# Kernel tuning notes

Measured on AMD Instinct MI355X. Metric: run time of the kernel, lower is better.

## Reference

```python
import jax, jax.numpy as jnp
import numpy as np

EPS_ATTN = 1e-5   # attention denominator eps (module eps)
EPS_LN = 1e-5     # nn.LayerNorm default eps


def _prime(x, proj):
    # Performer FAVOR+ hyperbolic positive features.
    # x: (B,H,L,dh), proj: (dh,m) -> (B,H,L,2m)
    dn = x.shape[-1] ** -0.25
    xn = dn * x
    d = jnp.einsum('bhld,dm->bhlm', xn, proj)
    diag = 0.5 * jnp.sum(xn * xn, axis=-1, keepdims=True)
    return jnp.concatenate([jnp.exp(d - diag), jnp.exp(-d - diag)], axis=-1)


def setup_inputs() -> dict:
    L, B, H, DH, DM, M = 2048, 4, 8, 64, 512, 256
    key = jax.random.key(0)
    k0, k1, k2 = jax.random.split(key, 3)
    h = jax.random.normal(k0, (L, B, DM), jnp.float32)
    w_qkv = jax.random.normal(k1, (H * 3 * DH, DM), jnp.float32) / np.sqrt(DM)
    w_o = jax.random.normal(k2, (DM, H * DH), jnp.float32) / np.sqrt(H * DH)
    ln_gamma = jnp.ones((DM,), jnp.float32)
    ln_beta = jnp.zeros((DM,), jnp.float32)
    # Gaussian orthogonal random matrix (blockwise QR), rows scaled by sqrt(dh)
    rng = np.random.default_rng(0)
    blocks = []
    for _ in range(M // DH):
        g = rng.standard_normal((DH, DH)).astype(np.float32)
        q, _ = np.linalg.qr(g)
        blocks.append(q.T)
    pm = np.concatenate(blocks, axis=0) * np.sqrt(DH)  # (M, DH)
    proj_matrix = jnp.asarray(pm.T.astype(np.float32))  # (DH, M)
    return {"h": h, "w_qkv": w_qkv, "w_o": w_o,
            "ln_gamma": ln_gamma, "ln_beta": ln_beta,
            "proj_matrix": proj_matrix}


def _forward(h, w_qkv, w_o, ln_gamma, ln_beta, proj_matrix):
    L, B, DM = h.shape
    DH, M = proj_matrix.shape
    H = w_qkv.shape[0] // (3 * DH)
    scale = DH ** -0.5

    qkv = (h @ w_qkv.T).reshape(L, B, H, 3 * DH)
    q, k, v = jnp.split(qkv, 3, axis=-1)
    q = jnp.transpose(q, (1, 2, 0, 3))  # (B,H,L,dh)
    k = jnp.transpose(k, (1, 2, 0, 3))
    v = jnp.transpose(v, (1, 2, 0, 3))

    qp = _prime(q, proj_matrix)  # (B,H,L,2M)
    kp = _prime(k, proj_matrix)
    kp = kp / jnp.sum(kp, axis=-1, keepdims=True)
    qp = qp / jnp.sum(qp, axis=-1, keepdims=True)

    den_acc = jnp.cumsum(kp, axis=2)
    denom = jnp.einsum('bhlm,bhlm->bhl', den_acc, qp)[..., None]  # (B,H,L,1)

    # fast_weight_sum: W_t = W_{t-1} + k_t v_t^T ; out_t = q_t @ W_t
    def step(W, xs):
        qt, kt, vt = xs  # (B,H,2M), (B,H,2M), (B,H,dh)
        W = W + kt[..., :, None] * vt[..., None, :]
        out = jnp.einsum('bhm,bhmd->bhd', qt, W)
        return W, out

    W0 = jnp.zeros((B, H, 2 * M, DH), h.dtype)
    xs = (jnp.transpose(qp, (2, 0, 1, 3)),
          jnp.transpose(kp, (2, 0, 1, 3)),
          jnp.transpose(v, (2, 0, 1, 3)))
    _, out = jax.lax.scan(step, W0, xs)  # (L,B,H,dh)
    out = jnp.transpose(out, (1, 2, 0, 3))  # (B,H,L,dh)

    out = scale * out / (denom + EPS_ATTN)
    out = jnp.transpose(out, (0, 2, 1, 3)).reshape(B, L, H * DH)  # (B,L,H*dh)
    out = jnp.swapaxes(out, 0, 1)  # (L,B,H*dh)

    attn_out = out @ w_o.T
    x = h + attn_out
    mu = jnp.mean(x, axis=-1, keepdims=True)
    var = jnp.mean((x - mu) ** 2, axis=-1, keepdims=True)
    return (x - mu) / jnp.sqrt(var + EPS_LN) * ln_gamma + ln_beta


def reference(h, w_qkv, w_o, ln_gamma, ln_beta, proj_matrix):
    return _forward(h, w_qkv, w_o, ln_gamma, ln_beta, proj_matrix)
```

## Files before the change

kernel.cpp:

```cpp
#include <hip/hip_runtime.h>
#include <hip/hip_fp16.h>
#include <math.h>

#define LSEQ 2048
#define NB 4
#define NH 8
#define DMID 512
#define CHK 128
#define SCALE 0.125f
#define DN 0.35355339059327373f
#define DN2 0.125f
#define EPS_ATTN 1e-5f
#define EPS_LN 1e-5f

typedef _Float16 f16x8 __attribute__((ext_vector_type(8)));
typedef _Float16 f16x4 __attribute__((ext_vector_type(4)));
typedef float f32x4 __attribute__((ext_vector_type(4)));

__device__ __forceinline__ void cvt16(const float* __restrict__ p,
                                      _Float16* __restrict__ dst) {
  float4 a = *(const float4*)p, b = *(const float4*)(p + 4);
  float4 c = *(const float4*)(p + 8), d = *(const float4*)(p + 12);
  f16x8 t0 = {(_Float16)a.x, (_Float16)a.y, (_Float16)a.z, (_Float16)a.w,
              (_Float16)b.x, (_Float16)b.y, (_Float16)b.z, (_Float16)b.w};
  f16x8 t1 = {(_Float16)c.x, (_Float16)c.y, (_Float16)c.z, (_Float16)c.w,
              (_Float16)d.x, (_Float16)d.y, (_Float16)d.z, (_Float16)d.w};
  *(f16x8*)dst = t0;
  *(f16x8*)(dst + 8) = t1;
}

__global__ void k_diag(float* out, int n, float val) {
  int i = blockIdx.x * 256 + threadIdx.x;
  if (i < n) out[i] = val;
}

__global__ __launch_bounds__(256) void k_ptr(const float* __restrict__ proj,
                                             __half* __restrict__ projT) {
  int e = blockIdx.x * 256 + threadIdx.x;
  int n = e >> 6, k = e & 63;
  projT[e] = __float2half_rn(proj[k * 256 + n] * DN);
}

__global__ __launch_bounds__(256) void k_qkv(
    const float* __restrict__ A, const float* __restrict__ Wq,
    __half* __restrict__ q, __half* __restrict__ k, __half* __restrict__ v) {
  __shared__ __align__(16) char smem[34816];
  _Float16* Ah = (_Float16*)smem;
  _Float16* Bh = (_Float16*)(smem + 10240);
  _Float16* Oh = (_Float16*)smem;

  const int tid = threadIdx.x;
  const int row0 = blockIdx.x * 128;
  const int col0 = blockIdx.y * 128;
  const int lane = tid & 63, wv = tid >> 6;
  const int ln15 = lane & 15, quad = lane >> 4;
  const int m0 = wv * 32;
  const int srow = tid >> 1, sc = (tid & 1) * 16;

  f32x4 Cacc[2][8];
  const f32x4 z4 = {0.f, 0.f, 0.f, 0.f};
#pragma unroll
  for (int mi = 0; mi < 2; ++mi)
#pragma unroll
    for (int nt = 0; nt < 8; ++nt) Cacc[mi][nt] = z4;

  for (int kt = 0; kt < DMID; kt += 32) {
    cvt16(A + (size_t)(row0 + srow) * DMID + kt + sc, &Ah[srow * 40 + sc]);
    cvt16(Wq + (size_t)(col0 + srow) * DMID + kt + sc, &Bh[srow * 40 + sc]);
    __syncthreads();
    f16x8 a0 = *(const f16x8*)&Ah[(m0 + ln15) * 40 + quad * 8];
    f16x8 a1 = *(const f16x8*)&Ah[(m0 + 16 + ln15) * 40 + quad * 8];
#pragma unroll
    for (int nt = 0; nt < 8; ++nt) {
      f16x8 bf = *(const f16x8*)&Bh[(nt * 16 + ln15) * 40 + quad * 8];
      Cacc[0][nt] = __builtin_amdgcn_mfma_f32_16x16x32_f16(a0, bf, Cacc[0][nt], 0, 0, 0);
      Cacc[1][nt] = __builtin_amdgcn_mfma_f32_16x16x32_f16(a1, bf, Cacc[1][nt], 0, 0, 0);
    }
    __syncthreads();
  }
#pragma unroll
  for (int mi = 0; mi < 2; ++mi)
#pragma unroll
    for (int nt = 0; nt < 8; ++nt)
#pragma unroll
      for (int r = 0; r < 4; ++r)
        Oh[(m0 + mi * 16 + quad * 4 + r) * 136 + nt * 16 + ln15] =
            (_Float16)Cacc[mi][nt][r];
  __syncthreads();
  const int tr = tid >> 4, tc = tid & 15;
  const int col = col0 + tc * 8;
  const int hh = col / 192;
  const int rem = col - hh * 192;
  const int t = rem >> 6;
  const int d0 = rem & 63;
  __half* dstb = (t == 0) ? q : ((t == 1) ? k : v);
#pragma unroll
  for (int i = 0; i < 8; ++i) {
    int lrow = tr * 8 + i;
    int grow = row0 + lrow;
    int l = grow >> 2, bb = grow & 3;
    f16x8 val = *(const f16x8*)&Oh[lrow * 136 + tc * 8];
    *(f16x8*)((_Float16*)dstb + (((size_t)(bb * NH + hh) * LSEQ + l) << 6) + d0) = val;
  }
}

__global__ __launch_bounds__(256, 4) void k_dgemm(
    const __half* __restrict__ qsrc, const __half* __restrict__ ksrc,
    const __half* __restrict__ projT, __half* __restrict__ dqd,
    __half* __restrict__ dkd, float2* __restrict__ nq,
    float2* __restrict__ nk) {
  __shared__ __align__(16) char smem[37376];
  _Float16* Bt = (_Float16*)smem;
  float* g_l  = (float*)(smem + 36864);
  float* ps_l = (float*)(smem + 37120);
  _Float16* Oh = (_Float16*)smem;

  const int tid = threadIdx.x;
  const __half* src = blockIdx.y ? ksrc : qsrc;
  __half* dst = blockIdx.y ? dkd : dqd;
  float2* nrm = blockIdx.y ? nk : nq;
  const size_t r0 = (size_t)blockIdx.x * 64;

  const int lane = tid & 63, wv = tid >> 6;
  const int ln15 = lane & 15, quad = lane >> 4;
  const int m0 = wv * 16;

#pragma unroll
  for (int it = 0; it < 8; ++it) {
    int e = it * 256 + tid;
    int n = e >> 3, seg = e & 7;
    *(f16x8*)&Bt[n * 72 + seg * 8] =
        *(const f16x8*)((const _Float16*)projT + n * 64 + seg * 8);
  }

  f16x8 afrag[2];
  float ss = 0.f;
  {
    const _Float16* rp = (const _Float16*)src + (r0 + m0 + ln15) * 64;
#pragma unroll
    for (int ks = 0; ks < 2; ++ks) {
      f16x8 x8 = *(const f16x8*)(rp + ks * 32 + quad * 8);
      afrag[ks] = x8;
#pragma unroll
      for (int j = 0; j < 8; ++j) {
        float xv = (float)x8[j];
        ss = fmaf(xv, xv, ss);
      }
    }
    ss += __shfl_xor(ss, 16);
    ss += __shfl_xor(ss, 32);
  }
  if (quad == 0) g_l[m0 + ln15] = 0.5f * DN2 * ss;
  __syncthreads();

  f32x4 Cacc[16];
  const f32x4 z4 = {0.f, 0.f, 0.f, 0.f};
#pragma unroll
  for (int nt = 0; nt < 16; ++nt) Cacc[nt] = z4;

#pragma unroll
  for (int ks = 0; ks < 2; ++ks) {
    f16x8 a0 = afrag[ks];
#pragma unroll
    for (int nt = 0; nt < 16; ++nt) {
      f16x8 bf = *(const f16x8*)&Bt[(nt * 16 + ln15) * 72 + ks * 32 + quad * 8];
      Cacc[nt] = __builtin_amdgcn_mfma_f32_16x16x32_f16(a0, bf, Cacc[nt], 0, 0, 0);
    }
  }

  float gv[4], pp[4];
#pragma unroll
  for (int r = 0; r < 4; ++r) {
    gv[r] = g_l[m0 + quad * 4 + r];
    pp[r] = 0.f;
  }
#pragma unroll
  for (int nt = 0; nt < 16; ++nt)
#pragma unroll
    for (int r = 0; r < 4; ++r) {
      float d = Cacc[nt][r];
      pp[r] += __expf(d - gv[r]) + __expf(-d - gv[r]);
    }
#pragma unroll
  for (int r = 0; r < 4; ++r) {
    float p = pp[r];
    p += __shfl_xor(p, 1); p += __shfl_xor(p, 2);
    p += __shfl_xor(p, 4); p += __shfl_xor(p, 8);
    if (ln15 == 0) ps_l[m0 + quad * 4 + r] = p;
  }

#pragma unroll
  for (int hf = 0; hf < 2; ++hf) {
    __syncthreads();
#pragma unroll
    for (int nt2 = 0; nt2 < 8; ++nt2) {
      int nt = hf * 8 + nt2;
#pragma unroll
      for (int r = 0; r < 4; ++r)
        Oh[(m0 + quad * 4 + r) * 136 + nt2 * 16 + ln15] =
            (_Float16)Cacc[nt][r];
    }
    __syncthreads();
#pragma unroll
    for (int it = 0; it < 4; ++it) {
      int e = it * 256 + tid;
      int row = e >> 4, seg = e & 15;
      *(f16x8*)((_Float16*)dst + (r0 + row) * 256 + hf * 128 + seg * 8) =
          *(const f16x8*)&Oh[row * 136 + seg * 8];
    }
  }
  if (tid < 64) nrm[r0 + tid] = make_float2(g_l[tid], 1.0f / ps_l[tid]);
}

__global__ __launch_bounds__(256) void k_kv(
    const __half* __restrict__ dk, const float2* __restrict__ nk,
    const __half* __restrict__ v, __half* __restrict__ KVt,
    float* __restrict__ Ks) {
  __shared__ __align__(16) char smem[53248];
  _Float16* kpT = (_Float16*)smem;
  _Float16* Vt  = (_Float16*)(smem + 34816);
  float* gk = (float*)(smem + 52224);
  float* ik = (float*)(smem + 52736);
  _Float16* Oh2 = (_Float16*)smem;

  const int tid = threadIdx.x;
  const int cidx = blockIdx.x;
  const int i0 = blockIdx.y * 128;
  const float fsign = (i0 < 256) ? 1.f : -1.f;
  const int m0col = (i0 < 256) ? i0 : i0 - 256;
  const size_t rowbase = (size_t)cidx * CHK;

  if (tid < 128) {
    float2 n = nk[rowbase + tid];
    gk[tid] = n.x; ik[tid] = n.y;
  }
  __syncthreads();

  {
    const int srow = tid >> 1;
    const int scol = (tid & 1) * 64;
    float g = gk[srow], ivs = ik[srow];
    const _Float16* src =
        (const _Float16*)dk + (rowbase + srow) * 256 + m0col + scol;
#pragma unroll
    for (int it = 0; it < 8; ++it) {
      f16x8 d8 = *(const f16x8*)(src + it * 8);
#pragma unroll
      for (int j = 0; j < 8; ++j)
        kpT[(scol + it * 8 + j) * 136 + srow] =
            (_Float16)(__expf(fsign * (float)d8[j] - g) * ivs);
    }
  }
  {
    int s = tid & 127, dq0 = (tid >> 7) * 32;
    const _Float16* vsrc = (const _Float16*)v + (rowbase + s) * 64 + dq0;
#pragma unroll
    for (int b8 = 0; b8 < 4; ++b8) {
      f16x8 v8 = ((const f16x8*)vsrc)[b8];
#pragma unroll
      for (int j = 0; j < 8; ++j)
        Vt[(dq0 + b8 * 8 + j) * 136 + s] = v8[j];
    }
  }
  __syncthreads();

  const int lane = tid & 63, wv = tid >> 6;
  const int ln15 = lane & 15, quad = lane >> 4;
  const int m0 = wv * 32;

  f32x4 Cacc[2][4], Kacc[2];
  const f32x4 z4 = {0.f, 0.f, 0.f, 0.f};
#pragma unroll
  for (int mi = 0; mi < 2; ++mi) {
#pragma unroll
    for (int nt = 0; nt < 4; ++nt) Cacc[mi][nt] = z4;
    Kacc[mi] = z4;
  }
  f16x8 bone;
#pragma unroll
  for (int j = 0; j < 8; ++j)
    bone[j] = (ln15 == 0) ? (_Float16)1.0f : (_Float16)0.0f;

#pragma unroll
  for (int ks = 0; ks < 4; ++ks) {
    f16x8 a0 = *(const f16x8*)&kpT[(m0 + ln15) * 136 + ks * 32 + quad * 8];
    f16x8 a1 = *(const f16x8*)&kpT[(m0 + 16 + ln15) * 136 + ks * 32 + quad * 8];
#pragma unroll
    for (int nt = 0; nt < 4; ++nt) {
      f16x8 bV = *(const f16x8*)&Vt[(nt * 16 + ln15) * 136 + ks * 32 + quad * 8];
      Cacc[0][nt] = __builtin_amdgcn_mfma_f32_16x16x32_f16(a0, bV, Cacc[0][nt], 0, 0, 0);
      Cacc[1][nt] = __builtin_amdgcn_mfma_f32_16x16x32_f16(a1, bV, Cacc[1][nt], 0, 0, 0);
    }
    Kacc[0] = __builtin_amdgcn_mfma_f32_16x16x32_f16(a0, bone, Kacc[0], 0, 0, 0);
    Kacc[1] = __builtin_amdgcn_mfma_f32_16x16x32_f16(a1, bone, Kacc[1], 0, 0, 0);
  }

  if (ln15 == 0) {
#pragma unroll
    for (int mi = 0; mi < 2; ++mi)
#pragma unroll
      for (int r = 0; r < 4; ++r)
        Ks[(size_t)cidx * 512 + i0 + m0 + mi * 16 + quad * 4 + r] = Kacc[mi][r];
  }
  __syncthreads();
#pragma unroll
  for (int mi = 0; mi < 2; ++mi)
#pragma unroll
    for (int nt = 0; nt < 4; ++nt) {
      f16x4 pack = {(_Float16)Cacc[mi][nt][0], (_Float16)Cacc[mi][nt][1],
                    (_Float16)Cacc[mi][nt][2], (_Float16)Cacc[mi][nt][3]};
      *(f16x4*)&Oh2[(nt * 16 + ln15) * 136 + m0 + mi * 16 + quad * 4] = pack;
    }
  __syncthreads();
  {
    int d = tid >> 2, part = tid & 3;
    _Float16* dstp =
        (_Float16*)KVt + (size_t)cidx * 32768 + d * 512 + i0 + part * 32;
    const _Float16* srcp = &Oh2[d * 136 + part * 32];
#pragma unroll
    for (int j = 0; j < 4; ++j)
      *(f16x8*)(dstp + j * 8) = *(const f16x8*)(srcp + j * 8);
  }
}

__global__ __launch_bounds__(256) void k_scan(__half2* __restrict__ KV2,
                                              float* __restrict__ Ks) {
  const int bh = blockIdx.x;
  const int e0 = blockIdx.y * 2048;
  for (int ee = 0; ee < 8; ++ee) {
    int e = e0 + ee * 256 + threadIdx.x;
    float ax = 0.f, ay = 0.f;
    __half2* p = KV2 + (size_t)bh * 16 * 16384 + e;
#pragma unroll
    for (int c = 0; c < 16; ++c) {
      float2 f = __half22float2(p[(size_t)c * 16384]);
      p[(size_t)c * 16384] = __floats2half2_rn(ax, ay);
      ax += f.x; ay += f.y;
    }
  }
  if (blockIdx.y == 0) {
    for (int ee = 0; ee < 2; ++ee) {
      int i = ee * 256 + threadIdx.x;
      float a = 0.f;
      float* p = Ks + (size_t)bh * 16 * 512 + i;
#pragma unroll
      for (int c = 0; c < 16; ++c) {
        float vv = p[c * 512];
        p[c * 512] = a;
        a += vv;
      }
    }
  }
}

template <int TH>
__device__ __forceinline__ void attn_body(
    const __half* __restrict__ dq, const __half* __restrict__ dk,
    const float2* __restrict__ nq, const float2* __restrict__ nk,
    const __half* __restrict__ v, const __half* __restrict__ KVt,
    const float* __restrict__ Kpre, float* __restrict__ outb, char* smem) {
  constexpr int KROWS = TH ? 128 : 64;
  constexpr int NS = TH ? 8 : 4;
  constexpr int NKS = TH ? 4 : 2;

  float* gq_l   = (float*)(smem);
  float* iq_l   = (float*)(smem + 256);
  float* gk_l   = (float*)(smem + 512);
  float* ik_l   = (float*)(smem + 1024);
  float* den1_l = (float*)(smem + 1536);
  float* den2_l = (float*)(smem + 1792);
  float* invd_l = (float*)(smem + 2048);
  float* KpT    = (float*)(smem + 2304);
  _Float16* qpT = (_Float16*)(smem + 2432);
  _Float16* kpT = (_Float16*)(smem + 7552);
  _Float16* WT  = (_Float16*)(smem + 17792);
  _Float16* S_h = (_Float16*)(smem + 2432);
  _Float16* Vt  = (_Float16*)(smem + 22912);

  const int tid = threadIdx.x;
  const int cidx = blockIdx.x;
  const int cc = cidx & 15, bh = cidx >> 4;
  const size_t rowb = (size_t)cidx * 128;
  const size_t rowt = rowb + TH * 64;
  const int lane = tid & 63;
  const int wv = tid >> 6;
  const int ln15 = lane & 15;
  const int quad = lane >> 4;
  const int m0 = wv * 16;

  if (tid < 64) {
    float2 n = nq[rowt + tid];
    gq_l[tid] = n.x; iq_l[tid] = n.y;
  }
  if (tid < KROWS) {
    float2 n2 = nk[rowb + tid];
    gk_l[tid] = n2.x; ik_l[tid] = n2.y;
  }
  __syncthreads();

  f32x4 Sacc[NS], Oacc[4], Dacc;
  const f32x4 z4 = {0.f, 0.f, 0.f, 0.f};
#pragma unroll
  for (int nt = 0; nt < NS; ++nt) Sacc[nt] = z4;
#pragma unroll
  for (int nt = 0; nt < 4; ++nt) Oacc[nt] = z4;
  Dacc = z4;

  const int qrow = tid >> 2, qc = (tid & 3) * 8;
  const int krow = tid >> 1, kc = (tid & 1) * 16;

  for (int kt = 0; kt < 512; kt += 32) {
    const float sgn = (kt < 256) ? 1.f : -1.f;
    const int dbase = (kt < 256) ? kt : kt - 256;
    {
      const _Float16* src = (const _Float16*)dq + (rowt + qrow) * 256 + dbase + qc;
      float g = gq_l[qrow], iv = iq_l[qrow];
      f16x8 d0 = *(const f16x8*)(src);
      f16x8 t0;
#pragma unroll
      for (int j = 0; j < 8; ++j)
        t0[j] = (_Float16)(__expf(sgn * (float)d0[j] - g) * iv);
      *(f16x8*)&qpT[qrow * 40 + qc] = t0;
    }
    if (TH == 1 || krow < 64) {
      const _Float16* src = (const _Float16*)dk + (rowb + krow) * 256 + dbase + kc;
      float g = gk_l[krow], iv = ik_l[krow];
      f16x8 d0 = *(const f16x8*)(src);
      f16x8 d1 = *(const f16x8*)(src + 8);
      f16x8 t0, t1;
#pragma unroll
      for (int j = 0; j < 8; ++j) {
        t0[j] = (_Float16)(__expf(sgn * (float)d0[j] - g) * iv);
        t1[j] = (_Float16)(__expf(sgn * (float)d1[j] - g) * iv);
      }
      *(f16x8*)&kpT[krow * 40 + kc] = t0;
      *(f16x8*)&kpT[krow * 40 + kc + 8] = t1;
    }
    {
      int d = tid >> 2, seg = tid & 3;
      *(f16x8*)&WT[d * 40 + seg * 8] =
          *(const f16x8*)((const _Float16*)KVt + (size_t)cidx * 32768 +
                          d * 512 + kt + seg * 8);
    }
    if (tid < 32) KpT[tid] = Kpre[(size_t)cidx * 512 + kt + tid];
    __syncthreads();

    f16x8 a0 = *(const f16x8*)&qpT[(m0 + ln15) * 40 + quad * 8];
#pragma unroll
    for (int nt = 0; nt < NS; ++nt) {
      f16x8 bf = *(const f16x8*)&kpT[(nt * 16 + ln15) * 40 + quad * 8];
      Sacc[nt] = __builtin_amdgcn_mfma_f32_16x16x32_f16(a0, bf, Sacc[nt], 0, 0, 0);
    }
#pragma unroll
    for (int nt = 0; nt < 4; ++nt) {
      f16x8 bw = *(const f16x8*)&WT[(nt * 16 + ln15) * 40 + quad * 8];
      Oacc[nt] = __builtin_amdgcn_mfma_f32_16x16x32_f16(a0, bw, Oacc[nt], 0, 0, 0);
    }
    {
      f16x8 bk;
#pragma unroll
      for (int j = 0; j < 8; ++j)
        bk[j] = (ln15 == 0) ? (_Float16)KpT[quad * 8 + j] : (_Float16)0.f;
      Dacc = __builtin_amdgcn_mfma_f32_16x16x32_f16(a0, bk, Dacc, 0, 0, 0);
    }
    __syncthreads();
  }

  if (ln15 == 0) {
#pragma unroll
    for (int r = 0; r < 4; ++r)
      den2_l[m0 + quad * 4 + r] = Dacc[r];
  }
  {
    float dp[4] = {0.f, 0.f, 0.f, 0.f};
#pragma unroll
    for (int nt = 0; nt < NS; ++nt) {
      int s = nt * 16 + ln15;
#pragma unroll
      for (int r = 0; r < 4; ++r) {
        int tl = m0 + quad * 4 + r;
        float vsv = (s <= TH * 64 + tl) ? Sacc[nt][r] : 0.f;
        dp[r] += vsv;
        S_h[tl * 136 + s] = (_Float16)vsv;
      }
    }
#pragma unroll
    for (int r = 0; r < 4; ++r) {
      float p = dp[r];
      p += __shfl_xor(p, 1); p += __shfl_xor(p, 2);
      p += __shfl_xor(p, 4); p += __shfl_xor(p, 8);
      if (ln15 == 0) den1_l[m0 + quad * 4 + r] = p;
    }
  }
  __syncthreads();
  if (tid < 64)
    invd_l[tid] = SCALE / (den1_l[tid] + den2_l[tid] + EPS_ATTN);
  {
    int s = tid & 127, d0v = (tid >> 7) * 32;
    if (TH == 1 || s < 64) {
      const _Float16* vsrc = (const _Float16*)v + (rowb + s) * 64 + d0v;
      f16x8 v0 = ((const f16x8*)vsrc)[0];
      f16x8 v1 = ((const f16x8*)vsrc)[1];
      f16x8 v2 = ((const f16x8*)vsrc)[2];
      f16x8 v3 = ((const f16x8*)vsrc)[3];
#pragma unroll
      for (int j = 0; j < 8; ++j) {
        Vt[(d0v + j) * 136 + s] = v0[j];
        Vt[(d0v + 8 + j) * 136 + s] = v1[j];
        Vt[(d0v + 16 + j) * 136 + s] = v2[j];
        Vt[(d0v + 24 + j) * 136 + s] = v3[j];
      }
    }
  }
  __syncthreads();
#pragma unroll
  for (int ks = 0; ks < NKS; ++ks) {
    f16x8 aS0 = *(const f16x8*)&S_h[(m0 + ln15) * 136 + ks * 32 + quad * 8];
#pragma unroll
    for (int nt = 0; nt < 4; ++nt) {
      f16x8 bV = *(const f16x8*)&Vt[(nt * 16 + ln15) * 136 + ks * 32 + quad * 8];
      Oacc[nt] = __builtin_amdgcn_mfma_f32_16x16x32_f16(aS0, bV, Oacc[nt], 0, 0, 0);
    }
  }
  const int b = bh >> 3, hh = bh & 7;
  float ivv[4];
#pragma unroll
  for (int r = 0; r < 4; ++r)
    ivv[r] = invd_l[m0 + quad * 4 + r];
#pragma unroll
  for (int nt = 0; nt < 4; ++nt) {
    int dcol = nt * 16 + ln15;
#pragma unroll
    for (int r = 0; r < 4; ++r) {
      int tl = m0 + quad * 4 + r;
      int l = cc * 128 + TH * 64 + tl;
      outb[((size_t)l * 4 + b) * 512 + hh * 64 + dcol] = Oacc[nt][r] * ivv[r];
    }
  }
}

__global__ __launch_bounds__(256, 4) void k_attn(
    const __half* __restrict__ dq, const __half* __restrict__ dk,
    const float2* __restrict__ nq, const float2* __restrict__ nk,
    const __half* __restrict__ v, const __half* __restrict__ KVt,
    const float* __restrict__ Kpre, float* __restrict__ outb) {
  __shared__ __align__(16) char smem[40320];
  if (blockIdx.y == 0)
    attn_body<0>(dq, dk, nq, nk, v, KVt, Kpre, outb, smem);
  else
    attn_body<1>(dq, dk, nq, nk, v, KVt, Kpre, outb, smem);
}

__global__ __launch_bounds__(256) void k_oproj(
    const float* __restrict__ A, const float* __restrict__ Wo,
    const float* __restrict__ hres, float* __restrict__ xout) {
  __shared__ __align__(16) char smem[34816];
  _Float16* Ah = (_Float16*)smem;
  _Float16* Bh = (_Float16*)(smem + 10240);
  _Float16* Oh = (_Float16*)smem;

  const int tid = threadIdx.x;
  const int row0 = blockIdx.x * 128;
  const int col0 = blockIdx.y * 128;
  const int lane = tid & 63, wv = tid >> 6;
  const int ln15 = lane & 15, quad = lane >> 4;
  const int m0 = wv * 32;
  const int srow = tid >> 1, sc = (tid & 1) * 16;

  f32x4 Cacc[2][8];
  const f32x4 z4 = {0.f, 0.f, 0.f, 0.f};
#pragma unroll
  for (int mi = 0; mi < 2; ++mi)
#pragma unroll
    for (int nt = 0; nt < 8; ++nt) Cacc[mi][nt] = z4;

  for (int kt = 0; kt < DMID; kt += 32) {
    cvt16(A + (size_t)(row0 + srow) * DMID + kt + sc, &Ah[srow * 40 + sc]);
    cvt16(Wo + (size_t)(col0 + srow) * DMID + kt + sc, &Bh[srow * 40 + sc]);
    __syncthreads();
    f16x8 a0 = *(const f16x8*)&Ah[(m0 + ln15) * 40 + quad * 8];
    f16x8 a1 = *(const f16x8*)&Ah[(m0 + 16 + ln15) * 40 + quad * 8];
#pragma unroll
    for (int nt = 0; nt < 8; ++nt) {
      f16x8 bf = *(const f16x8*)&Bh[(nt * 16 + ln15) * 40 + quad * 8];
      Cacc[0][nt] = __builtin_amdgcn_mfma_f32_16x16x32_f16(a0, bf, Cacc[0][nt], 0, 0, 0);
      Cacc[1][nt] = __builtin_amdgcn_mfma_f32_16x16x32_f16(a1, bf, Cacc[1][nt], 0, 0, 0);
    }
    __syncthreads();
  }
#pragma unroll
  for (int mi = 0; mi < 2; ++mi)
#pragma unroll
    for (int nt = 0; nt < 8; ++nt)
#pragma unroll
      for (int r = 0; r < 4; ++r)
        Oh[(m0 + mi * 16 + quad * 4 + r) * 136 + nt * 16 + ln15] =
            (_Float16)Cacc[mi][nt][r];
  __syncthreads();
  const int tr = tid >> 4, tc = tid & 15;
#pragma unroll
  for (int i = 0; i < 8; ++i) {
    int lrow = tr * 8 + i;
    int grow = row0 + lrow;
    size_t base = (size_t)grow * 512 + col0 + tc * 8;
    f16x8 o = *(const f16x8*)&Oh[lrow * 136 + tc * 8];
    float4 h0 = *(const float4*)(hres + base);
    float4 h1 = *(const float4*)(hres + base + 4);
    *(float4*)(xout + base) =
        make_float4((float)o[0] + h0.x, (float)o[1] + h0.y,
                    (float)o[2] + h0.z, (float)o[3] + h0.w);
    *(float4*)(xout + base + 4) =
        make_float4((float)o[4] + h1.x, (float)o[5] + h1.y,
                    (float)o[6] + h1.z, (float)o[7] + h1.w);
  }
}

__global__ __launch_bounds__(256) void k_ln(float* __restrict__ x,
                                            const float* __restrict__ g,
                                            const float* __restrict__ bta) {
  __shared__ float ws_[4], wq_[4];
  const int row = blockIdx.x;
  const int tid = threadIdx.x;
  float2 vv = *(const float2*)(x + (size_t)row * 512 + tid * 2);
  float s = vv.x + vv.y;
  float sq = vv.x * vv.x + vv.y * vv.y;
#pragma unroll
  for (int off = 1; off < 64; off <<= 1) {
    s += __shfl_xor(s, off, 64);
    sq += __shfl_xor(sq, off, 64);
  }
  if ((tid & 63) == 0) { ws_[tid >> 6] = s; wq_[tid >> 6] = sq; }
  __syncthreads();
  s = ws_[0] + ws_[1] + ws_[2] + ws_[3];
  sq = wq_[0] + wq_[1] + wq_[2] + wq_[3];
  float mu = s * (1.f / 512.f);
  float var = sq * (1.f / 512.f) - mu * mu;
  float rstd = rsqrtf(var + EPS_LN);
  int c = tid * 2;
  float2 o;
  o.x = (vv.x - mu) * rstd * g[c] + bta[c];
  o.y = (vv.y - mu) * rstd * g[c + 1] + bta[c + 1];
  *(float2*)(x + (size_t)row * 512 + c) = o;
}

extern "C" void kernel_launch(void* const* d_in, const int* in_sizes, int n_in,
                              void* d_out, int out_size, void* d_ws,
                              size_t ws_size, hipStream_t stream) {
  const float* h    = (const float*)d_in[0];
  const float* wqkv = (const float*)d_in[1];
  const float* wo   = (const float*)d_in[2];
  const float* g    = (const float*)d_in[3];
  const float* bta  = (const float*)d_in[4];
  const float* proj = (const float*)d_in[5];
  float* out = (float*)d_out;
  char* wsb = (char*)d_ws;

  __half* q   = (__half*)(wsb + 0);
  __half* kb  = (__half*)(wsb + 8388608);
  __half* vb  = (__half*)(wsb + 16777216);
  __half* dq  = (__half*)(wsb + 25165824);
  __half* dk  = (__half*)(wsb + 58720256);
  float2* nq  = (float2*)(wsb + 92274688);
  float2* nk  = (float2*)(wsb + 92798976);
  __half* KVt = (__half*)(wsb + 93323264);
  float*  Ks  = (float*)(wsb + 126877696);
  __half* pT  = (__half*)(wsb + 127926272);
  float* outb = (float*)(wsb + 0);

  if (ws_size < 127959040ull) {
    float val = 1000.0f + (float)(ws_size >> 20);
    k_diag<<<(out_size + 255) / 256, 256, 0, stream>>>(out, out_size, val);
    return;
  }

  k_ptr  <<<dim3(64), 256, 0, stream>>>(proj, pT);
  k_qkv  <<<dim3(64, 12), 256, 0, stream>>>(h, wqkv, q, kb, vb);
  k_dgemm<<<dim3(1024, 2), 256, 0, stream>>>(q, kb, pT, dq, dk, nq, nk);
  k_kv   <<<dim3(512, 4), 256, 0, stream>>>(dk, nk, vb, KVt, Ks);
  k_scan <<<dim3(32, 8), 256, 0, stream>>>((__half2*)KVt, Ks);
  k_attn <<<dim3(512, 2), 256, 0, stream>>>(dq, dk, nq, nk, vb, KVt, Ks, outb);
  k_oproj<<<dim3(64, 4), 256, 0, stream>>>(outb, wo, h, out);
  k_ln   <<<dim3(8192), 256, 0, stream>>>(out, g, bta);
}
```

Before: 257.6 us.

## Register-prefetch attention tiles, widen k-step, parallelize scan, remap attn blocks

The attention kernel now handles 64 feature columns per iteration instead of 32, giving 8 iterations rather than 16. It prefetches the next tile's dq, dk, KV and Kpre values into registers while the current tile is computed, which hides global-load latency and halves the number of barriers. The chunk scan is split across more blocks: each thread does vectorized 8-byte loads of all 16 chunks up front, and the Ks prefix sum runs in separate blocks. The attention grid is flattened and remapped so that the two halves of a chunk run in adjacent blocks, which may improve cache locality. The costs are higher register pressure and a changed shared-memory layout.

```diff
diff --git a/kernel.cpp b/kernel.cpp
--- a/kernel.cpp
+++ b/kernel.cpp
@@ -326,30 +326,35 @@
 __global__ __launch_bounds__(256) void k_scan(__half2* __restrict__ KV2,
                                               float* __restrict__ Ks) {
   const int bh = blockIdx.x;
-  const int e0 = blockIdx.y * 2048;
-  for (int ee = 0; ee < 8; ++ee) {
-    int e = e0 + ee * 256 + threadIdx.x;
-    float ax = 0.f, ay = 0.f;
-    __half2* p = KV2 + (size_t)bh * 16 * 16384 + e;
+  const int tid = threadIdx.x;
+  if (blockIdx.y < 32) {
+    uint2* p = (uint2*)(KV2 + (size_t)bh * 262144) + (blockIdx.y * 256 + tid);
+    uint2 raw[16];
+#pragma unroll
+    for (int c = 0; c < 16; ++c) raw[c] = p[c * 8192];
+    float ax0 = 0.f, ay0 = 0.f, ax1 = 0.f, ay1 = 0.f;
 #pragma unroll
     for (int c = 0; c < 16; ++c) {
-      float2 f = __half22float2(p[(size_t)c * 16384]);
-      p[(size_t)c * 16384] = __floats2half2_rn(ax, ay);
-      ax += f.x; ay += f.y;
-    }
-  }
-  if (blockIdx.y == 0) {
-    for (int ee = 0; ee < 2; ++ee) {
-      int i = ee * 256 + threadIdx.x;
-      float a = 0.f;
-      float* p = Ks + (size_t)bh * 16 * 512 + i;
-#pragma unroll
-      for (int c = 0; c < 16; ++c) {
-        float vv = p[c * 512];
-        p[c * 512] = a;
-        a += vv;
-      }
-    }
+      __half2 h0 = *(__half2*)&raw[c].x;
+      __half2 h1 = *(__half2*)&raw[c].y;
+      float2 f0 = __half22float2(h0), f1 = __half22float2(h1);
+      __half2 o0 = __floats2half2_rn(ax0, ay0);
+      __half2 o1 = __floats2half2_rn(ax1, ay1);
+      uint2 o;
+      o.x = *(unsigned*)&o0;
+      o.y = *(unsigned*)&o1;
+      p[c * 8192] = o;
+      ax0 += f0.x; ay0 += f0.y; ax1 += f1.x; ay1 += f1.y;
+    }
+  } else {
+    int i = (blockIdx.y - 32) * 256 + tid;
+    float* pk = Ks + (size_t)bh * 8192 + i;
+    float vs[16];
+#pragma unroll
+    for (int c = 0; c < 16; ++c) vs[c] = pk[c * 512];
+    float a = 0.f;
+#pragma unroll
+    for (int c = 0; c < 16; ++c) { pk[c * 512] = a; a += vs[c]; }
   }
 }
 
@@ -358,27 +363,28 @@
     const __half* __restrict__ dq, const __half* __restrict__ dk,
     const float2* __restrict__ nq, const float2* __restrict__ nk,
     const __half* __restrict__ v, const __half* __restrict__ KVt,
-    const float* __restrict__ Kpre, float* __restrict__ outb, char* smem) {
+    const float* __restrict__ Kpre, float* __restrict__ outb, int cidx,
+    char* smem) {
   constexpr int KROWS = TH ? 128 : 64;
+  constexpr int KR32 = KROWS / 32;
   constexpr int NS = TH ? 8 : 4;
   constexpr int NKS = TH ? 4 : 2;
 
-  float* gq_l   = (float*)(smem);
-  float* iq_l   = (float*)(smem + 256);
-  float* gk_l   = (float*)(smem + 512);
-  float* ik_l   = (float*)(smem + 1024);
-  float* den1_l = (float*)(smem + 1536);
-  float* den2_l = (float*)(smem + 1792);
-  float* invd_l = (float*)(smem + 2048);
-  float* KpT    = (float*)(smem + 2304);
-  _Float16* qpT = (_Float16*)(smem + 2432);
-  _Float16* kpT = (_Float16*)(smem + 7552);
-  _Float16* WT  = (_Float16*)(smem + 17792);
-  _Float16* S_h = (_Float16*)(smem + 2432);
-  _Float16* Vt  = (_Float16*)(smem + 22912);
+  _Float16* qpT = (_Float16*)(smem);
+  _Float16* kpT = (_Float16*)(smem + 9216);
+  _Float16* WT  = (_Float16*)(smem + 27648);
+  float*    KpT = (float*)(smem + 36864);
+  _Float16* S_h = (_Float16*)(smem);
+  _Float16* Vt  = (_Float16*)(smem + 17408);
+  float* gq_l   = (float*)(smem + 37120);
+  float* iq_l   = (float*)(smem + 37376);
+  float* gk_l   = (float*)(smem + 37632);
+  float* ik_l   = (float*)(smem + 38144);
+  float* den1_l = (float*)(smem + 38656);
+  float* den2_l = (float*)(smem + 38912);
+  float* invd_l = (float*)(smem + 39168);
 
   const int tid = threadIdx.x;
-  const int cidx = blockIdx.x;
   const int cc = cidx & 15, bh = cidx >> 4;
   const size_t rowb = (size_t)cidx * 128;
   const size_t rowt = rowb + TH * 64;
@@ -398,6 +404,40 @@
   }
   __syncthreads();
 
+  const int c8 = tid & 7;
+  const int r8 = tid >> 3;
+  const int csrc = (c8 & 3) * 8;
+  const float sgn = (c8 < 4) ? 1.f : -1.f;
+
+  const _Float16* qsrc = (const _Float16*)dq + (rowt + r8) * 256 + csrc;
+  const _Float16* ksrc = (const _Float16*)dk + (rowb + r8) * 256 + csrc;
+  const _Float16* wsrc = (const _Float16*)KVt + (size_t)cidx * 32768 +
+                         r8 * 512 + ((c8 < 4) ? 0 : 256) + csrc;
+  const float* kpsrc = Kpre + (size_t)cidx * 512 +
+                       ((tid < 32) ? tid : (tid < 64 ? 224 + tid : 0));
+
+  float gq[2], iq[2], gk[KR32], ik[KR32];
+#pragma unroll
+  for (int p = 0; p < 2; ++p) {
+    gq[p] = gq_l[r8 + p * 32];
+    iq[p] = iq_l[r8 + p * 32];
+  }
+#pragma unroll
+  for (int p = 0; p < KR32; ++p) {
+    gk[p] = gk_l[r8 + p * 32];
+    ik[p] = ik_l[r8 + p * 32];
+  }
+
+  f16x8 rq[2], rk[KR32], rw[2];
+  float rkp = 0.f;
+#pragma unroll
+  for (int p = 0; p < 2; ++p) rq[p] = *(const f16x8*)(qsrc + p * 8192);
+#pragma unroll
+  for (int p = 0; p < KR32; ++p) rk[p] = *(const f16x8*)(ksrc + p * 8192);
+#pragma unroll
+  for (int p = 0; p < 2; ++p) rw[p] = *(const f16x8*)(wsrc + p * 16384);
+  if (tid < 64) rkp = kpsrc[0];
+
   f32x4 Sacc[NS], Oacc[4], Dacc;
   const f32x4 z4 = {0.f, 0.f, 0.f, 0.f};
 #pragma unroll
@@ -406,61 +446,61 @@
   for (int nt = 0; nt < 4; ++nt) Oacc[nt] = z4;
   Dacc = z4;
 
-  const int qrow = tid >> 2, qc = (tid & 3) * 8;
-  const int krow = tid >> 1, kc = (tid & 1) * 16;
-
-  for (int kt = 0; kt < 512; kt += 32) {
-    const float sgn = (kt < 256) ? 1.f : -1.f;
-    const int dbase = (kt < 256) ? kt : kt - 256;
-    {
-      const _Float16* src = (const _Float16*)dq + (rowt + qrow) * 256 + dbase + qc;
-      float g = gq_l[qrow], iv = iq_l[qrow];
-      f16x8 d0 = *(const f16x8*)(src);
-      f16x8 t0;
+  for (int it = 0; it < 8; ++it) {
+#pragma unroll
+    for (int p = 0; p < 2; ++p) {
+      f16x8 d = rq[p], t;
 #pragma unroll
       for (int j = 0; j < 8; ++j)
-        t0[j] = (_Float16)(__expf(sgn * (float)d0[j] - g) * iv);
-      *(f16x8*)&qpT[qrow * 40 + qc] = t0;
-    }
-    if (TH == 1 || krow < 64) {
-      const _Float16* src = (const _Float16*)dk + (rowb + krow) * 256 + dbase + kc;
-      float g = gk_l[krow], iv = ik_l[krow];
-      f16x8 d0 = *(const f16x8*)(src);
-      f16x8 d1 = *(const f16x8*)(src + 8);
-      f16x8 t0, t1;
-#pragma unroll
-      for (int j = 0; j < 8; ++j) {
-        t0[j] = (_Float16)(__expf(sgn * (float)d0[j] - g) * iv);
-        t1[j] = (_Float16)(__expf(sgn * (float)d1[j] - g) * iv);
+        t[j] = (_Float16)(__expf(sgn * (float)d[j] - gq[p]) * iq[p]);
+      *(f16x8*)&qpT[(r8 + p * 32) * 72 + c8 * 8] = t;
+    }
+#pragma unroll
+    for (int p = 0; p < KR32; ++p) {
+      f16x8 d = rk[p], t;
+#pragma unroll
+      for (int j = 0; j < 8; ++j)
+        t[j] = (_Float16)(__expf(sgn * (float)d[j] - gk[p]) * ik[p]);
+      *(f16x8*)&kpT[(r8 + p * 32) * 72 + c8 * 8] = t;
+    }
+#pragma unroll
+    for (int p = 0; p < 2; ++p)
+      *(f16x8*)&WT[(r8 + p * 32) * 72 + c8 * 8] = rw[p];
+    if (tid < 64) KpT[tid] = rkp;
+
+    if (it < 7) {
+      const int nb = (it + 1) * 32;
+#pragma unroll
+      for (int p = 0; p < 2; ++p)
+        rq[p] = *(const f16x8*)(qsrc + p * 8192 + nb);
+#pragma unroll
+      for (int p = 0; p < KR32; ++p)
+        rk[p] = *(const f16x8*)(ksrc + p * 8192 + nb);
+#pragma unroll
+      for (int p = 0; p < 2; ++p)
+        rw[p] = *(const f16x8*)(wsrc + p * 16384 + nb);
+      if (tid < 64) rkp = kpsrc[nb];
+    }
+    __syncthreads();
+
+#pragma unroll
+    for (int ks = 0; ks < 2; ++ks) {
+      f16x8 a0 = *(const f16x8*)&qpT[(m0 + ln15) * 72 + ks * 32 + quad * 8];
+#pragma unroll
+      for (int nt = 0; nt < NS; ++nt) {
+        f16x8 bf = *(const f16x8*)&kpT[(nt * 16 + ln15) * 72 + ks * 32 + quad * 8];
+        Sacc[nt] = __builtin_amdgcn_mfma_f32_16x16x32_f16(a0, bf, Sacc[nt], 0, 0, 0);
       }
-      *(f16x8*)&kpT[krow * 40 + kc] = t0;
-      *(f16x8*)&kpT[krow * 40 + kc + 8] = t1;
-    }
-    {
-      int d = tid >> 2, seg = tid & 3;
-      *(f16x8*)&WT[d * 40 + seg * 8] =
-          *(const f16x8*)((const _Float16*)KVt + (size_t)cidx * 32768 +
-                          d * 512 + kt + seg * 8);
-    }
-    if (tid < 32) KpT[tid] = Kpre[(size_t)cidx * 512 + kt + tid];
-    __syncthreads();
-
-    f16x8 a0 = *(const f16x8*)&qpT[(m0 + ln15) * 40 + quad * 8];
-#pragma unroll
-    for (int nt = 0; nt < NS; ++nt) {
-      f16x8 bf = *(const f16x8*)&kpT[(nt * 16 + ln15) * 40 + quad * 8];
-      Sacc[nt] = __builtin_amdgcn_mfma_f32_16x16x32_f16(a0, bf, Sacc[nt], 0, 0, 0);
-    }
-#pragma unroll
-    for (int nt = 0; nt < 4; ++nt) {
-      f16x8 bw = *(const f16x8*)&WT[(nt * 16 + ln15) * 40 + quad * 8];
-      Oacc[nt] = __builtin_amdgcn_mfma_f32_16x16x32_f16(a0, bw, Oacc[nt], 0, 0, 0);
-    }
-    {
+#pragma unroll
+      for (int nt = 0; nt < 4; ++nt) {
+        f16x8 bw = *(const f16x8*)&WT[(nt * 16 + ln15) * 72 + ks * 32 + quad * 8];
+        Oacc[nt] = __builtin_amdgcn_mfma_f32_16x16x32_f16(a0, bw, Oacc[nt], 0, 0, 0);
+      }
       f16x8 bk;
 #pragma unroll
       for (int j = 0; j < 8; ++j)
-        bk[j] = (ln15 == 0) ? (_Float16)KpT[quad * 8 + j] : (_Float16)0.f;
+        bk[j] = (ln15 == 0) ? (_Float16)KpT[ks * 32 + quad * 8 + j]
+                            : (_Float16)0.f;
       Dacc = __builtin_amdgcn_mfma_f32_16x16x32_f16(a0, bk, Dacc, 0, 0, 0);
     }
     __syncthreads();
@@ -544,11 +584,13 @@
     const float2* __restrict__ nq, const float2* __restrict__ nk,
     const __half* __restrict__ v, const __half* __restrict__ KVt,
     const float* __restrict__ Kpre, float* __restrict__ outb) {
-  __shared__ __align__(16) char smem[40320];
-  if (blockIdx.y == 0)
-    attn_body<0>(dq, dk, nq, nk, v, KVt, Kpre, outb, smem);
+  __shared__ __align__(16) char smem[39424];
+  const int bid = blockIdx.x;
+  const int cidx = ((bid >> 4) << 3) + (bid & 7);
+  if (((bid >> 3) & 1) == 0)
+    attn_body<0>(dq, dk, nq, nk, v, KVt, Kpre, outb, cidx, smem);
   else
-    attn_body<1>(dq, dk, nq, nk, v, KVt, Kpre, outb, smem);
+    attn_body<1>(dq, dk, nq, nk, v, KVt, Kpre, outb, cidx, smem);
 }
 
 __global__ __launch_bounds__(256) void k_oproj(
@@ -677,8 +719,8 @@
   k_qkv  <<<dim3(64, 12), 256, 0, stream>>>(h, wqkv, q, kb, vb);
   k_dgemm<<<dim3(1024, 2), 256, 0, stream>>>(q, kb, pT, dq, dk, nq, nk);
   k_kv   <<<dim3(512, 4), 256, 0, stream>>>(dk, nk, vb, KVt, Ks);
-  k_scan <<<dim3(32, 8), 256, 0, stream>>>((__half2*)KVt, Ks);
-  k_attn <<<dim3(512, 2), 256, 0, stream>>>(dq, dk, nq, nk, vb, KVt, Ks, outb);
+  k_scan <<<dim3(32, 34), 256, 0, stream>>>((__half2*)KVt, Ks);
+  k_attn <<<dim3(1024), 256, 0, stream>>>(dq, dk, nq, nk, vb, KVt, Ks, outb);
   k_oproj<<<dim3(64, 4), 256, 0, stream>>>(outb, wo, h, out);
   k_ln   <<<dim3(8192), 256, 0, stream>>>(out, g, bta);
 }
```

Result: slower. 269.1 us (+4.5%).
